# Kernel optimization log

Measured on AMD Instinct MI355X. Metric: run time of the kernel, lower is better.

## Reference

```python
import jax, jax.numpy as jnp
import numpy as np

NUM_SPLITS = 2  # attn_splits


def _split_c_last(x, ns):
    # split_feature(channel_last=True): [b,h,w,c] -> [b*ns*ns, h/ns, w/ns, c]
    b, h, w, c = x.shape
    x = x.reshape(b, ns, h // ns, ns, w // ns, c)
    x = jnp.transpose(x, (0, 1, 3, 2, 4, 5))
    return x.reshape(b * ns * ns, h // ns, w // ns, c)


def _merge_c_last(x, ns):
    # merge_splits(channel_last=True): [b*ns*ns, hh, ww, c] -> [b, ns*hh, ns*ww, c]
    bn, hh, ww, c = x.shape
    b = bn // (ns * ns)
    x = x.reshape(b, ns, ns, hh, ww, c)
    x = jnp.transpose(x, (0, 1, 3, 2, 4, 5))
    return x.reshape(b, ns * hh, ns * ww, c)


def _make_shift_window_mask(h, w, ns):
    # exact port of generate_shift_window_attn_mask (numpy, setup-time only)
    wh, ww = h // ns, w // ns
    sh, sw = wh // 2, ww // 2
    img = np.zeros((h, w))
    cnt = 0
    for hs in (slice(0, -wh), slice(-wh, -sh), slice(-sh, None)):
        for ws in (slice(0, -ww), slice(-ww, -sw), slice(-sw, None)):
            img[hs, ws] = cnt
            cnt += 1
    mw = img.reshape(ns, wh, ns, ww).transpose(0, 2, 1, 3).reshape(ns * ns, wh * ww)
    am = mw[:, None, :] - mw[:, :, None]  # [n, i, j] = mw[n, j] - mw[n, i]
    am = np.where(am != 0, -100.0, 0.0).astype(np.float32)
    return jnp.asarray(am)


def _window_attention(q, k, v, attn_mask, h, w, ns):
    # single_head_split_window_attention with with_shift=True
    b, hw, c = q.shape
    sh, sw = (h // ns) // 2, (w // ns) // 2

    def prep(x):
        x = x.reshape(b, h, w, c)
        x = jnp.roll(x, shift=(-sh, -sw), axis=(1, 2))
        return _split_c_last(x, ns).reshape(b * ns * ns, -1, c)

    qs, ks, vs = prep(q), prep(k), prep(v)
    scale = jnp.asarray(c, q.dtype) ** 0.5
    scores = jnp.einsum('bqc,bkc->bqk', qs, ks) / scale
    scores = scores + jnp.tile(attn_mask, (b, 1, 1))
    attn = jax.nn.softmax(scores, axis=-1)
    out = jnp.einsum('bqk,bkc->bqc', attn, vs)
    out = _merge_c_last(out.reshape(b * ns * ns, h // ns, w // ns, c), ns)
    out = jnp.roll(out, shift=(sh, sw), axis=(1, 2))
    return out.reshape(b, hw, c)


def _global_correlation_softmax(feature0, feature1):
    b, c, h, w = feature0.shape
    hw = h * w
    f0 = feature0.reshape(b, c, hw).transpose(0, 2, 1)  # [b, hw, c]
    f1 = feature1.reshape(b, c, hw)                     # [b, c, hw]
    scale = jnp.asarray(c, feature0.dtype) ** 0.5
    corr = jnp.matmul(f0, f1) / scale                   # [b, hw, hw]

    yy, xx = jnp.meshgrid(jnp.arange(h), jnp.arange(w), indexing='ij')
    init_grid = jnp.stack([xx, yy], axis=0).astype(feature0.dtype)  # [2,h,w]
    init_grid = jnp.broadcast_to(init_grid[None], (b, 2, h, w))
    grid = init_grid.reshape(b, 2, hw).transpose(0, 2, 1)            # [b, hw, 2]

    corr2 = jnp.concatenate([corr, jnp.transpose(corr, (0, 2, 1))], axis=0)  # [2b,hw,hw]
    grid2 = jnp.tile(grid, (2, 1, 1))
    init2 = jnp.tile(init_grid, (2, 1, 1, 1))

    prob = jax.nn.softmax(corr2, axis=-1)
    corresp = jnp.matmul(prob, grid2).reshape(2 * b, h, w, 2)
    corresp = jnp.transpose(corresp, (0, 3, 1, 2))
    flow = corresp - init2
    f01, f10 = flow[:b], flow[b:]
    dual_prob = prob[:b] * jnp.transpose(prob[b:], (0, 2, 1))
    return f01, f10, dual_prob


def setup_inputs() -> dict:
    key = jax.random.key(0)
    b, c, h, w = 2, 128, 48, 96
    ks = jax.random.split(key, 5)
    q = jax.random.normal(ks[0], (b, h * w, c), dtype=jnp.float32)
    k = jax.random.normal(ks[1], (b, h * w, c), dtype=jnp.float32)
    v = jax.random.normal(ks[2], (b, h * w, c), dtype=jnp.float32)
    feature0 = jax.random.normal(ks[3], (b, c, h, w), dtype=jnp.float32)
    feature1 = jax.random.normal(ks[4], (b, c, h, w), dtype=jnp.float32)
    attn_mask = _make_shift_window_mask(h, w, NUM_SPLITS)
    return {"q": q, "k": k, "v": v, "feature0": feature0, "feature1": feature1,
            "attn_mask": attn_mask, "h": h, "w": w}


def reference(q, k, v, feature0, feature1, attn_mask, h, w):
    attn_out = _window_attention(q, k, v, attn_mask, h, w, NUM_SPLITS)
    f01, f10, dual_prob = _global_correlation_softmax(feature0, feature1)
    return (attn_out, f01, f10, dual_prob)
```

## Files before the change

kernel.cpp:

```cpp
#include <hip/hip_runtime.h>

#define HW 4608
#define CC 128
#define H 48
#define W 96
#define S_WIN 1152
#define SCALE 0.08838834764831845f

typedef __attribute__((ext_vector_type(8))) short bf16x8;
typedef __attribute__((ext_vector_type(4))) float f32x4;

static __device__ inline short f2bf(float f) {
    unsigned u = __builtin_bit_cast(unsigned, f);
    unsigned r = (u + 0x7fff + ((u >> 16) & 1)) >> 16;
    return (short)r;
}

__global__ __launch_bounds__(256)
void prep_corr(const float* __restrict__ f0, const float* __restrict__ f1,
               bf16x8* __restrict__ fragA, bf16x8* __restrict__ fragB)
{
    __shared__ float vt[32][68];
    const int t = threadIdx.x;
    const int pt = blockIdx.x;
    const int z  = blockIdx.y;
    const int tensor = z >> 3, b = (z >> 2) & 1, kc = z & 3;
    const float* src = (tensor ? f1 : f0) + (size_t)b * CC * HW + (size_t)kc * 32 * HW + pt * 64;
    {
        int ch = t >> 4;
        int c4 = (t & 15) * 4;
        *(float4*)&vt[ch][c4]      = *(const float4*)&src[(size_t)ch * HW + c4];
        *(float4*)&vt[ch + 16][c4] = *(const float4*)&src[(size_t)(ch + 16) * HW + c4];
    }
    __syncthreads();
    int Rloc = t >> 6, lane = t & 63;
    int R = pt * 4 + Rloc;
    bf16x8 v;
    #pragma unroll
    for (int j = 0; j < 8; ++j) v[j] = f2bf(vt[(lane >> 4) * 8 + j][Rloc * 16 + (lane & 15)]);
    (tensor ? fragB : fragA)[((size_t)(b * 288 + R) * 4 + kc) * 64 + lane] = v;
}

__global__ __launch_bounds__(256)
void prep_qkv(const float* __restrict__ Q, const float* __restrict__ K, const float* __restrict__ V,
              bf16x8* __restrict__ qfrag, bf16x8* __restrict__ kfrag, bf16x8* __restrict__ vfrag)
{
    __shared__ float vt[32][132];
    const int t  = threadIdx.x;
    const int R2 = blockIdx.x;
    const int z  = blockIdx.y;
    const int tensor = z >> 3, wb = z & 7;
    const int bb = wb >> 2, wi = wb & 3, si = wi >> 1, sj = wi & 1;
    const float* src = (tensor == 0 ? Q : (tensor == 1 ? K : V)) + (size_t)bb * HW * CC;
    {
        int row = t >> 3;
        int c16 = (t & 7) * 16;
        int qw = R2 * 32 + row;
        int rr = qw / 48, cc = qw - rr * 48;
        int y = (si * 24 + rr + 12) % 48;
        int x = (sj * 48 + cc + 24) % 96;
        const float* rp = src + ((size_t)y * 96 + x) * CC + c16;
        #pragma unroll
        for (int u = 0; u < 4; ++u)
            *(float4*)&vt[row][c16 + u * 4] = *(const float4*)&rp[u * 4];
    }
    __syncthreads();
    if (tensor < 2) {
        bf16x8* frag = tensor == 0 ? qfrag : kfrag;
        #pragma unroll
        for (int e2 = 0; e2 < 2; ++e2) {
            int e = t + e2 * 256;
            int Rloc = e >> 8, kc = (e >> 6) & 3, lane = e & 63;
            int R = R2 * 2 + Rloc;
            bf16x8 v;
            #pragma unroll
            for (int j = 0; j < 8; ++j)
                v[j] = f2bf(vt[Rloc * 16 + (lane & 15)][kc * 32 + (lane >> 4) * 8 + j]);
            frag[((size_t)(wb * 72 + R) * 4 + kc) * 64 + lane] = v;
        }
    } else {
        #pragma unroll
        for (int e2 = 0; e2 < 2; ++e2) {
            int e = t + e2 * 256;
            int dB = e >> 6, lane = e & 63;
            bf16x8 v;
            #pragma unroll
            for (int j = 0; j < 8; ++j)
                v[j] = f2bf(vt[(lane >> 4) * 8 + j][dB * 16 + (lane & 15)]);
            vfrag[((size_t)(wb * 8 + dB) * 36 + R2) * 64 + lane] = v;
        }
    }
}

__global__ __launch_bounds__(512)
void win_attn(const bf16x8* __restrict__ qfrag, const bf16x8* __restrict__ kfrag,
              const bf16x8* __restrict__ vfrag, float* __restrict__ out)
{
    __shared__ __align__(16) short Psh[32 * 1152];
    __shared__ unsigned char codes[S_WIN];
    __shared__ float rsum_sh[32];

    const int t = threadIdx.x, lane = t & 63, w = t >> 6;
    const int qt = blockIdx.x, wb = blockIdx.y;
    const int bb = wb >> 2, wi = wb & 3, si = wi >> 1, sj = wi & 1;

    if (t < 32) rsum_sh[t] = 0.f;
    for (int i = t; i < S_WIN; i += 512) {
        int r = i / 48, c = i - r * 48;
        int rb = si ? (r >= 12) : 0;
        int cb = sj ? (c >= 24) : 0;
        codes[i] = (unsigned char)(rb | (cb << 1));
    }
    __syncthreads();

    bf16x8 qf[2][4];
    {
        const bf16x8* qb = qfrag + ((size_t)(wb * 72 + qt * 2) * 4) * 64 + lane;
        #pragma unroll
        for (int qh = 0; qh < 2; ++qh)
            #pragma unroll
            for (int kc = 0; kc < 4; ++kc) qf[qh][kc] = qb[(qh * 4 + kc) * 64];
    }
    int qcode[2];
    qcode[0] = codes[qt * 32 + (lane & 15)];
    qcode[1] = codes[qt * 32 + 16 + (lane & 15)];

    char* Pb = (char*)Psh;
    float rsum[2] = {0.f, 0.f};

    for (int kt = 0; kt < 9; ++kt) {
        int Rk = w * 9 + kt;
        bf16x8 kf[4];
        const bf16x8* kb = kfrag + ((size_t)(wb * 72 + Rk) * 4) * 64 + lane;
        #pragma unroll
        for (int kc = 0; kc < 4; ++kc) kf[kc] = kb[kc * 64];
        int k0 = Rk * 16 + (lane >> 4) * 4;
        int kcd[4];
        #pragma unroll
        for (int r = 0; r < 4; ++r) kcd[r] = codes[k0 + r];
        #pragma unroll
        for (int qh = 0; qh < 2; ++qh) {
            f32x4 acc = {0.f, 0.f, 0.f, 0.f};
            #pragma unroll
            for (int kc = 0; kc < 4; ++kc)
                acc = __builtin_amdgcn_mfma_f32_16x16x32_bf16(kf[kc], qf[qh][kc], acc, 0, 0, 0);
            float ev[4];
            #pragma unroll
            for (int r = 0; r < 4; ++r) {
                ev[r] = (kcd[r] == qcode[qh]) ? __expf(acc[r] * SCALE) : 0.f;
                rsum[qh] += ev[r];
            }
            unsigned lo = (unsigned)(unsigned short)f2bf(ev[0]) | ((unsigned)(unsigned short)f2bf(ev[1]) << 16);
            unsigned hi = (unsigned)(unsigned short)f2bf(ev[2]) | ((unsigned)(unsigned short)f2bf(ev[3]) << 16);
            int qloc = qh * 16 + (lane & 15);
            int off = (qloc * 2304 + k0 * 2) ^ ((qloc & 7) << 4);
            *(uint2*)(Pb + off) = make_uint2(lo, hi);
        }
    }
    #pragma unroll
    for (int qh = 0; qh < 2; ++qh) {
        float s = rsum[qh];
        s += __shfl_xor(s, 16); s += __shfl_xor(s, 32);
        if (lane < 16) atomicAdd(&rsum_sh[qh * 16 + lane], s);
    }
    __syncthreads();

    f32x4 pv[2] = {};
    const bf16x8* vb = vfrag + ((size_t)(wb * 8 + w) * 36) * 64 + lane;
    for (int kc = 0; kc < 36; ++kc) {
        bf16x8 vf = vb[kc * 64];
        #pragma unroll
        for (int qh = 0; qh < 2; ++qh) {
            int qloc = qh * 16 + (lane & 15);
            int off = (qloc * 2304 + kc * 64 + (lane >> 4) * 16) ^ ((qloc & 7) << 4);
            bf16x8 pf = *(const bf16x8*)(Pb + off);
            pv[qh] = __builtin_amdgcn_mfma_f32_16x16x32_bf16(pf, vf, pv[qh], 0, 0, 0);
        }
    }
    #pragma unroll
    for (int qh = 0; qh < 2; ++qh) {
        #pragma unroll
        for (int r = 0; r < 4; ++r) {
            int qloc = qh * 16 + (lane >> 4) * 4 + r;
            float val = pv[qh][r] / rsum_sh[qloc];
            int qw = qt * 32 + qloc;
            int rr = qw / 48, cc2 = qw - rr * 48;
            int y = (si * 24 + rr + 12) % 48;
            int x = (sj * 48 + cc2 + 24) % 96;
            out[((size_t)bb * HW + y * 96 + x) * CC + w * 16 + (lane & 15)] = val;
        }
    }
}

__global__ __launch_bounds__(256)
void corr_stats(const bf16x8* __restrict__ fragA, const bf16x8* __restrict__ fragB,
                float* __restrict__ rowsum, float* __restrict__ colsum)
{
    __shared__ float rs[128], cs[128];
    const int t = threadIdx.x, lane = t & 63, wave = t >> 6;
    const int wm = wave >> 1, wn = wave & 1;
    const int kt = blockIdx.x, qt = blockIdx.y, b = blockIdx.z;

    const bf16x8* Ab = fragA + (size_t)(b * 288 + qt * 8 + wm * 4) * 256 + lane;
    const bf16x8* Bb = fragB + (size_t)(b * 288 + kt * 8 + wn * 4) * 256 + lane;

    f32x4 acc[4][4] = {};
    #pragma unroll
    for (int kc = 0; kc < 4; ++kc) {
        bf16x8 a[4], bf[4];
        #pragma unroll
        for (int m = 0; m < 4; ++m) a[m]  = Ab[(m * 4 + kc) * 64];
        #pragma unroll
        for (int n = 0; n < 4; ++n) bf[n] = Bb[(n * 4 + kc) * 64];
        #pragma unroll
        for (int m = 0; m < 4; ++m)
            #pragma unroll
            for (int n = 0; n < 4; ++n)
                acc[m][n] = __builtin_amdgcn_mfma_f32_16x16x32_bf16(a[m], bf[n], acc[m][n], 0, 0, 0);
    }

    if (t < 128) { rs[t] = 0.f; cs[t] = 0.f; }
    __syncthreads();

    float cv[4] = {};
    #pragma unroll
    for (int m = 0; m < 4; ++m) {
        float rv[4] = {};
        #pragma unroll
        for (int n = 0; n < 4; ++n)
            #pragma unroll
            for (int r = 0; r < 4; ++r) {
                float ev = __expf(acc[m][n][r] * SCALE);
                rv[r] += ev; cv[n] += ev;
            }
        #pragma unroll
        for (int r = 0; r < 4; ++r) {
            float s = rv[r];
            s += __shfl_xor(s, 1); s += __shfl_xor(s, 2);
            s += __shfl_xor(s, 4); s += __shfl_xor(s, 8);
            if ((lane & 15) == 0)
                atomicAdd(&rs[wm * 64 + m * 16 + (lane >> 4) * 4 + r], s);
        }
    }
    #pragma unroll
    for (int n = 0; n < 4; ++n) {
        float s = cv[n];
        s += __shfl_xor(s, 16); s += __shfl_xor(s, 32);
        if (lane < 16) atomicAdd(&cs[wn * 64 + n * 16 + lane], s);
    }
    __syncthreads();
    if (t < 128)      atomicAdd(&rowsum[(size_t)b * HW + qt * 128 + t], rs[t]);
    else              atomicAdd(&colsum[(size_t)b * HW + kt * 128 + (t - 128)], cs[t - 128]);
}

__global__ __launch_bounds__(256)
void corr_final(const bf16x8* __restrict__ fragA, const bf16x8* __restrict__ fragB,
                const float* __restrict__ rowsum, const float* __restrict__ colsum,
                float* __restrict__ rowflow, float* __restrict__ colflow,
                float* __restrict__ dual)
{
    __shared__ float sfx[128], sfy[128], scx[128], scy[128];
    const int t = threadIdx.x, lane = t & 63, wave = t >> 6;
    const int wm = wave >> 1, wn = wave & 1;
    const int kt = blockIdx.x, qt = blockIdx.y, b = blockIdx.z;

    const bf16x8* Ab = fragA + (size_t)(b * 288 + qt * 8 + wm * 4) * 256 + lane;
    const bf16x8* Bb = fragB + (size_t)(b * 288 + kt * 8 + wn * 4) * 256 + lane;

    f32x4 acc[4][4] = {};
    #pragma unroll
    for (int kc = 0; kc < 4; ++kc) {
        bf16x8 a[4], bf[4];
        #pragma unroll
        for (int m = 0; m < 4; ++m) a[m]  = Ab[(m * 4 + kc) * 64];
        #pragma unroll
        for (int n = 0; n < 4; ++n) bf[n] = Bb[(n * 4 + kc) * 64];
        #pragma unroll
        for (int m = 0; m < 4; ++m)
            #pragma unroll
            for (int n = 0; n < 4; ++n)
                acc[m][n] = __builtin_amdgcn_mfma_f32_16x16x32_bf16(a[m], bf[n], acc[m][n], 0, 0, 0);
    }

    if (t < 128) { sfx[t] = 0.f; sfy[t] = 0.f; scx[t] = 0.f; scy[t] = 0.f; }
    __syncthreads();

    const int qbase = qt * 128 + wm * 64;
    const int kbase = kt * 128 + wn * 64;

    float cinv[4], gkx[4], gky[4];
    #pragma unroll
    for (int n = 0; n < 4; ++n) {
        int k = kbase + n * 16 + (lane & 15);
        cinv[n] = 1.f / colsum[(size_t)b * HW + k];
        int kyi = k / W;
        gkx[n] = (float)(k - kyi * W); gky[n] = (float)kyi;
    }

    float cfx[4] = {}, cfy[4] = {};
    #pragma unroll
    for (int m = 0; m < 4; ++m) {
        float rinv[4], gqx[4], gqy[4];
        int q0 = qbase + m * 16 + (lane >> 4) * 4;
        #pragma unroll
        for (int r = 0; r < 4; ++r) {
            rinv[r] = 1.f / rowsum[(size_t)b * HW + q0 + r];
            int qyi = (q0 + r) / W;
            gqx[r] = (float)(q0 + r - qyi * W); gqy[r] = (float)qyi;
        }
        float rfx[4] = {}, rfy[4] = {};
        #pragma unroll
        for (int n = 0; n < 4; ++n) {
            #pragma unroll
            for (int r = 0; r < 4; ++r) {
                float ev = __expf(acc[m][n][r] * SCALE);
                float rp = ev * rinv[r];
                float ce = ev * cinv[n];
                dual[((size_t)b * HW + q0 + r) * HW + kbase + n * 16 + (lane & 15)] = rp * ce;
                rfx[r] += rp * gkx[n]; rfy[r] += rp * gky[n];
                cfx[n] += ce * gqx[r]; cfy[n] += ce * gqy[r];
            }
        }
        #pragma unroll
        for (int r = 0; r < 4; ++r) {
            float sx = rfx[r], sy = rfy[r];
            sx += __shfl_xor(sx, 1); sx += __shfl_xor(sx, 2);
            sx += __shfl_xor(sx, 4); sx += __shfl_xor(sx, 8);
            sy += __shfl_xor(sy, 1); sy += __shfl_xor(sy, 2);
            sy += __shfl_xor(sy, 4); sy += __shfl_xor(sy, 8);
            if ((lane & 15) == 0) {
                int row = wm * 64 + m * 16 + (lane >> 4) * 4 + r;
                atomicAdd(&sfx[row], sx); atomicAdd(&sfy[row], sy);
            }
        }
    }
    #pragma unroll
    for (int n = 0; n < 4; ++n) {
        float sx = cfx[n], sy = cfy[n];
        sx += __shfl_xor(sx, 16); sx += __shfl_xor(sx, 32);
        sy += __shfl_xor(sy, 16); sy += __shfl_xor(sy, 32);
        if (lane < 16) {
            int col = wn * 64 + n * 16 + lane;
            atomicAdd(&scx[col], sx); atomicAdd(&scy[col], sy);
        }
    }
    __syncthreads();
    if (t < 128) {
        atomicAdd(&rowflow[((size_t)b * HW + qt * 128 + t) * 2 + 0], sfx[t]);
        atomicAdd(&rowflow[((size_t)b * HW + qt * 128 + t) * 2 + 1], sfy[t]);
    } else {
        int j = t - 128;
        atomicAdd(&colflow[((size_t)b * HW + kt * 128 + j) * 2 + 0], scx[j]);
        atomicAdd(&colflow[((size_t)b * HW + kt * 128 + j) * 2 + 1], scy[j]);
    }
}

__global__ void flow_finalize(const float* __restrict__ rowflow, const float* __restrict__ colflow,
                              float* __restrict__ out)
{
    int i = blockIdx.x * 256 + threadIdx.x;
    if (i >= 2 * 2 * HW) return;
    int bb   = i / (2 * HW);
    int rem  = i % (2 * HW);
    int chan = rem / HW;
    int q    = rem % HW;
    float g = (chan == 0) ? (float)(q % W) : (float)(q / W);
    out[i]              = rowflow[((size_t)bb * HW + q) * 2 + chan] - g;
    out[2 * 2 * HW + i] = colflow[((size_t)bb * HW + q) * 2 + chan] - g;
}

extern "C" void kernel_launch(void* const* d_in, const int* in_sizes, int n_in,
                              void* d_out, int out_size, void* d_ws, size_t ws_size,
                              hipStream_t stream)
{
    (void)in_sizes; (void)n_in; (void)out_size; (void)ws_size;
    const float* q    = (const float*)d_in[0];
    const float* k    = (const float*)d_in[1];
    const float* v    = (const float*)d_in[2];
    const float* f0   = (const float*)d_in[3];
    const float* f1   = (const float*)d_in[4];

    float* out = (float*)d_out;
    const size_t ATTN_SZ = (size_t)2 * HW * CC;
    const size_t FLOW_SZ = (size_t)2 * 2 * HW;
    float* f01  = out + ATTN_SZ;
    float* dual = out + ATTN_SZ + 2 * FLOW_SZ;

    const size_t FR = 2359296;
    char* wsb = (char*)d_ws;
    bf16x8* cfragA = (bf16x8*)(wsb);
    bf16x8* cfragB = (bf16x8*)(wsb + FR);
    bf16x8* qfrag  = (bf16x8*)(wsb + 2 * FR);
    bf16x8* kfrag  = (bf16x8*)(wsb + 3 * FR);
    bf16x8* vfrag  = (bf16x8*)(wsb + 4 * FR);
    float* wsf     = (float*)(wsb + 5 * FR);
    float* rowsum  = wsf;
    float* colsum  = wsf + 2 * HW;
    float* rowflow = wsf + 4 * HW;
    float* colflow = wsf + 8 * HW;
    hipMemsetAsync(wsf, 0, (size_t)12 * HW * sizeof(float), stream);

    prep_corr<<<dim3(72, 16), 256, 0, stream>>>(f0, f1, cfragA, cfragB);
    prep_qkv<<<dim3(36, 24), 256, 0, stream>>>(q, k, v, qfrag, kfrag, vfrag);
    win_attn<<<dim3(36, 8), 512, 0, stream>>>(qfrag, kfrag, vfrag, out);
    corr_stats<<<dim3(36, 36, 2), 256, 0, stream>>>(cfragA, cfragB, rowsum, colsum);
    corr_final<<<dim3(36, 36, 2), 256, 0, stream>>>(cfragA, cfragB, rowsum, colsum,
                                                    rowflow, colflow, dual);
    flow_finalize<<<dim3(72), 256, 0, stream>>>(rowflow, colflow, f01);
}
```

Baseline: 141.0 us.

## Fuse prep kernels with memset, split window attention finer, coalesce dual stores

Merges the two prep kernels and the workspace memset into one launch, which removes launch and memset overhead. Window attention now handles 16 queries per block instead of 32, doubling the grid to 576 blocks and halving LDS use, so more blocks can be resident. The cost is that K and V fragments are reloaded twice as often. The dual-probability output in corr_final is staged through shared memory so it can be written as coalesced float4 rows, replacing scattered scalar stores on the largest output.

```diff
diff --git a/kernel.cpp b/kernel.cpp
--- a/kernel.cpp
+++ b/kernel.cpp
@@ -17,77 +17,80 @@
 }
 
 __global__ __launch_bounds__(256)
-void prep_corr(const float* __restrict__ f0, const float* __restrict__ f1,
-               bf16x8* __restrict__ fragA, bf16x8* __restrict__ fragB)
-{
-    __shared__ float vt[32][68];
+void prep_all(const float* __restrict__ Q, const float* __restrict__ K, const float* __restrict__ V,
+              const float* __restrict__ f0, const float* __restrict__ f1,
+              bf16x8* __restrict__ cfragA, bf16x8* __restrict__ cfragB,
+              bf16x8* __restrict__ qfrag, bf16x8* __restrict__ kfrag, bf16x8* __restrict__ vfrag,
+              float* __restrict__ wsf)
+{
+    __shared__ float vt[32][132];
+    const int bx = blockIdx.x;
     const int t = threadIdx.x;
-    const int pt = blockIdx.x;
-    const int z  = blockIdx.y;
-    const int tensor = z >> 3, b = (z >> 2) & 1, kc = z & 3;
-    const float* src = (tensor ? f1 : f0) + (size_t)b * CC * HW + (size_t)kc * 32 * HW + pt * 64;
-    {
-        int ch = t >> 4;
-        int c4 = (t & 15) * 4;
-        *(float4*)&vt[ch][c4]      = *(const float4*)&src[(size_t)ch * HW + c4];
-        *(float4*)&vt[ch + 16][c4] = *(const float4*)&src[(size_t)(ch + 16) * HW + c4];
-    }
-    __syncthreads();
-    int Rloc = t >> 6, lane = t & 63;
-    int R = pt * 4 + Rloc;
-    bf16x8 v;
-    #pragma unroll
-    for (int j = 0; j < 8; ++j) v[j] = f2bf(vt[(lane >> 4) * 8 + j][Rloc * 16 + (lane & 15)]);
-    (tensor ? fragB : fragA)[((size_t)(b * 288 + R) * 4 + kc) * 64 + lane] = v;
-}
-
-__global__ __launch_bounds__(256)
-void prep_qkv(const float* __restrict__ Q, const float* __restrict__ K, const float* __restrict__ V,
-              bf16x8* __restrict__ qfrag, bf16x8* __restrict__ kfrag, bf16x8* __restrict__ vfrag)
-{
-    __shared__ float vt[32][132];
-    const int t  = threadIdx.x;
-    const int R2 = blockIdx.x;
-    const int z  = blockIdx.y;
-    const int tensor = z >> 3, wb = z & 7;
-    const int bb = wb >> 2, wi = wb & 3, si = wi >> 1, sj = wi & 1;
-    const float* src = (tensor == 0 ? Q : (tensor == 1 ? K : V)) + (size_t)bb * HW * CC;
-    {
-        int row = t >> 3;
-        int c16 = (t & 7) * 16;
-        int qw = R2 * 32 + row;
-        int rr = qw / 48, cc = qw - rr * 48;
-        int y = (si * 24 + rr + 12) % 48;
-        int x = (sj * 48 + cc + 24) % 96;
-        const float* rp = src + ((size_t)y * 96 + x) * CC + c16;
-        #pragma unroll
-        for (int u = 0; u < 4; ++u)
-            *(float4*)&vt[row][c16 + u * 4] = *(const float4*)&rp[u * 4];
-    }
-    __syncthreads();
-    if (tensor < 2) {
-        bf16x8* frag = tensor == 0 ? qfrag : kfrag;
-        #pragma unroll
-        for (int e2 = 0; e2 < 2; ++e2) {
-            int e = t + e2 * 256;
-            int Rloc = e >> 8, kc = (e >> 6) & 3, lane = e & 63;
-            int R = R2 * 2 + Rloc;
-            bf16x8 v;
-            #pragma unroll
-            for (int j = 0; j < 8; ++j)
-                v[j] = f2bf(vt[Rloc * 16 + (lane & 15)][kc * 32 + (lane >> 4) * 8 + j]);
-            frag[((size_t)(wb * 72 + R) * 4 + kc) * 64 + lane] = v;
-        }
+
+    if (bx < 1152) {
+        int zi = bx * 256 + t;
+        if (zi < 12 * HW) wsf[zi] = 0.f;
+        const int pt = bx % 72;
+        const int z  = bx / 72;
+        const int tensor = z >> 3, b = (z >> 2) & 1, kc = z & 3;
+        const float* src = (tensor ? f1 : f0) + (size_t)b * CC * HW + (size_t)kc * 32 * HW + pt * 64;
+        {
+            int ch = t >> 4;
+            int c4 = (t & 15) * 4;
+            *(float4*)&vt[ch][c4]      = *(const float4*)&src[(size_t)ch * HW + c4];
+            *(float4*)&vt[ch + 16][c4] = *(const float4*)&src[(size_t)(ch + 16) * HW + c4];
+        }
+        __syncthreads();
+        int Rloc = t >> 6, lane = t & 63;
+        int R = pt * 4 + Rloc;
+        bf16x8 v;
+        #pragma unroll
+        for (int j = 0; j < 8; ++j) v[j] = f2bf(vt[(lane >> 4) * 8 + j][Rloc * 16 + (lane & 15)]);
+        (tensor ? cfragB : cfragA)[((size_t)(b * 288 + R) * 4 + kc) * 64 + lane] = v;
     } else {
-        #pragma unroll
-        for (int e2 = 0; e2 < 2; ++e2) {
-            int e = t + e2 * 256;
-            int dB = e >> 6, lane = e & 63;
-            bf16x8 v;
-            #pragma unroll
-            for (int j = 0; j < 8; ++j)
-                v[j] = f2bf(vt[(lane >> 4) * 8 + j][dB * 16 + (lane & 15)]);
-            vfrag[((size_t)(wb * 8 + dB) * 36 + R2) * 64 + lane] = v;
+        const int bx2 = bx - 1152;
+        const int R2 = bx2 % 36;
+        const int z  = bx2 / 36;
+        const int tensor = z >> 3, wb = z & 7;
+        const int bb = wb >> 2, wi = wb & 3, si = wi >> 1, sj = wi & 1;
+        const float* src = (tensor == 0 ? Q : (tensor == 1 ? K : V)) + (size_t)bb * HW * CC;
+        {
+            int row = t >> 3;
+            int c16 = (t & 7) * 16;
+            int qw = R2 * 32 + row;
+            int rr = qw / 48, cc = qw - rr * 48;
+            int y = (si * 24 + rr + 12) % 48;
+            int x = (sj * 48 + cc + 24) % 96;
+            const float* rp = src + ((size_t)y * 96 + x) * CC + c16;
+            #pragma unroll
+            for (int u = 0; u < 4; ++u)
+                *(float4*)&vt[row][c16 + u * 4] = *(const float4*)&rp[u * 4];
+        }
+        __syncthreads();
+        if (tensor < 2) {
+            bf16x8* frag = tensor == 0 ? qfrag : kfrag;
+            #pragma unroll
+            for (int e2 = 0; e2 < 2; ++e2) {
+                int e = t + e2 * 256;
+                int Rloc = e >> 8, kc = (e >> 6) & 3, lane = e & 63;
+                int R = R2 * 2 + Rloc;
+                bf16x8 v;
+                #pragma unroll
+                for (int j = 0; j < 8; ++j)
+                    v[j] = f2bf(vt[Rloc * 16 + (lane & 15)][kc * 32 + (lane >> 4) * 8 + j]);
+                frag[((size_t)(wb * 72 + R) * 4 + kc) * 64 + lane] = v;
+            }
+        } else {
+            #pragma unroll
+            for (int e2 = 0; e2 < 2; ++e2) {
+                int e = t + e2 * 256;
+                int dB = e >> 6, lane = e & 63;
+                bf16x8 v;
+                #pragma unroll
+                for (int j = 0; j < 8; ++j)
+                    v[j] = f2bf(vt[(lane >> 4) * 8 + j][dB * 16 + (lane & 15)]);
+                vfrag[((size_t)(wb * 8 + dB) * 36 + R2) * 64 + lane] = v;
+            }
         }
     }
 }
@@ -96,99 +99,76 @@
 void win_attn(const bf16x8* __restrict__ qfrag, const bf16x8* __restrict__ kfrag,
               const bf16x8* __restrict__ vfrag, float* __restrict__ out)
 {
-    __shared__ __align__(16) short Psh[32 * 1152];
+    __shared__ __align__(16) short Psh[16 * 1152];
     __shared__ unsigned char codes[S_WIN];
-    __shared__ float rsum_sh[32];
+    __shared__ float rsum_sh[16];
 
     const int t = threadIdx.x, lane = t & 63, w = t >> 6;
-    const int qt = blockIdx.x, wb = blockIdx.y;
+    const int qt = blockIdx.x;
+    const int wb = blockIdx.y;
     const int bb = wb >> 2, wi = wb & 3, si = wi >> 1, sj = wi & 1;
 
-    if (t < 32) rsum_sh[t] = 0.f;
+    if (t < 16) rsum_sh[t] = 0.f;
     for (int i = t; i < S_WIN; i += 512) {
         int r = i / 48, c = i - r * 48;
-        int rb = si ? (r >= 12) : 0;
-        int cb = sj ? (c >= 24) : 0;
-        codes[i] = (unsigned char)(rb | (cb << 1));
-    }
-    __syncthreads();
-
-    bf16x8 qf[2][4];
+        codes[i] = (unsigned char)((si ? (r >= 12) : 0) | ((sj ? (c >= 24) : 0) << 1));
+    }
+    __syncthreads();
+
+    bf16x8 qf[4];
     {
-        const bf16x8* qb = qfrag + ((size_t)(wb * 72 + qt * 2) * 4) * 64 + lane;
-        #pragma unroll
-        for (int qh = 0; qh < 2; ++qh)
-            #pragma unroll
-            for (int kc = 0; kc < 4; ++kc) qf[qh][kc] = qb[(qh * 4 + kc) * 64];
-    }
-    int qcode[2];
-    qcode[0] = codes[qt * 32 + (lane & 15)];
-    qcode[1] = codes[qt * 32 + 16 + (lane & 15)];
-
+        const bf16x8* qb = qfrag + ((size_t)(wb * 72 + qt) * 4) * 64 + lane;
+        #pragma unroll
+        for (int kc = 0; kc < 4; ++kc) qf[kc] = qb[kc * 64];
+    }
+    const int qcode = codes[qt * 16 + (lane & 15)];
     char* Pb = (char*)Psh;
-    float rsum[2] = {0.f, 0.f};
+    float rsum = 0.f;
 
     for (int kt = 0; kt < 9; ++kt) {
         int Rk = w * 9 + kt;
+        const bf16x8* kb = kfrag + ((size_t)(wb * 72 + Rk) * 4) * 64 + lane;
         bf16x8 kf[4];
-        const bf16x8* kb = kfrag + ((size_t)(wb * 72 + Rk) * 4) * 64 + lane;
         #pragma unroll
         for (int kc = 0; kc < 4; ++kc) kf[kc] = kb[kc * 64];
         int k0 = Rk * 16 + (lane >> 4) * 4;
-        int kcd[4];
-        #pragma unroll
-        for (int r = 0; r < 4; ++r) kcd[r] = codes[k0 + r];
-        #pragma unroll
-        for (int qh = 0; qh < 2; ++qh) {
-            f32x4 acc = {0.f, 0.f, 0.f, 0.f};
-            #pragma unroll
-            for (int kc = 0; kc < 4; ++kc)
-                acc = __builtin_amdgcn_mfma_f32_16x16x32_bf16(kf[kc], qf[qh][kc], acc, 0, 0, 0);
-            float ev[4];
-            #pragma unroll
-            for (int r = 0; r < 4; ++r) {
-                ev[r] = (kcd[r] == qcode[qh]) ? __expf(acc[r] * SCALE) : 0.f;
-                rsum[qh] += ev[r];
-            }
-            unsigned lo = (unsigned)(unsigned short)f2bf(ev[0]) | ((unsigned)(unsigned short)f2bf(ev[1]) << 16);
-            unsigned hi = (unsigned)(unsigned short)f2bf(ev[2]) | ((unsigned)(unsigned short)f2bf(ev[3]) << 16);
-            int qloc = qh * 16 + (lane & 15);
-            int off = (qloc * 2304 + k0 * 2) ^ ((qloc & 7) << 4);
-            *(uint2*)(Pb + off) = make_uint2(lo, hi);
-        }
-    }
-    #pragma unroll
-    for (int qh = 0; qh < 2; ++qh) {
-        float s = rsum[qh];
-        s += __shfl_xor(s, 16); s += __shfl_xor(s, 32);
-        if (lane < 16) atomicAdd(&rsum_sh[qh * 16 + lane], s);
-    }
-    __syncthreads();
-
-    f32x4 pv[2] = {};
+        f32x4 acc = {0.f, 0.f, 0.f, 0.f};
+        #pragma unroll
+        for (int kc = 0; kc < 4; ++kc)
+            acc = __builtin_amdgcn_mfma_f32_16x16x32_bf16(kf[kc], qf[kc], acc, 0, 0, 0);
+        float ev[4];
+        #pragma unroll
+        for (int r = 0; r < 4; ++r) {
+            ev[r] = (codes[k0 + r] == qcode) ? __expf(acc[r] * SCALE) : 0.f;
+            rsum += ev[r];
+        }
+        unsigned lo = (unsigned)(unsigned short)f2bf(ev[0]) | ((unsigned)(unsigned short)f2bf(ev[1]) << 16);
+        unsigned hi = (unsigned)(unsigned short)f2bf(ev[2]) | ((unsigned)(unsigned short)f2bf(ev[3]) << 16);
+        int qloc = lane & 15;
+        int off = (qloc * 2304 + k0 * 2) ^ ((qloc & 7) << 4);
+        *(uint2*)(Pb + off) = make_uint2(lo, hi);
+    }
+    rsum += __shfl_xor(rsum, 16); rsum += __shfl_xor(rsum, 32);
+    if (lane < 16) atomicAdd(&rsum_sh[lane], rsum);
+    __syncthreads();
+
+    f32x4 pv = {0.f, 0.f, 0.f, 0.f};
     const bf16x8* vb = vfrag + ((size_t)(wb * 8 + w) * 36) * 64 + lane;
     for (int kc = 0; kc < 36; ++kc) {
-        bf16x8 vf = vb[kc * 64];
-        #pragma unroll
-        for (int qh = 0; qh < 2; ++qh) {
-            int qloc = qh * 16 + (lane & 15);
-            int off = (qloc * 2304 + kc * 64 + (lane >> 4) * 16) ^ ((qloc & 7) << 4);
-            bf16x8 pf = *(const bf16x8*)(Pb + off);
-            pv[qh] = __builtin_amdgcn_mfma_f32_16x16x32_bf16(pf, vf, pv[qh], 0, 0, 0);
-        }
-    }
-    #pragma unroll
-    for (int qh = 0; qh < 2; ++qh) {
-        #pragma unroll
-        for (int r = 0; r < 4; ++r) {
-            int qloc = qh * 16 + (lane >> 4) * 4 + r;
-            float val = pv[qh][r] / rsum_sh[qloc];
-            int qw = qt * 32 + qloc;
-            int rr = qw / 48, cc2 = qw - rr * 48;
-            int y = (si * 24 + rr + 12) % 48;
-            int x = (sj * 48 + cc2 + 24) % 96;
-            out[((size_t)bb * HW + y * 96 + x) * CC + w * 16 + (lane & 15)] = val;
-        }
+        int qloc = lane & 15;
+        int off = (qloc * 2304 + kc * 64 + (lane >> 4) * 16) ^ ((qloc & 7) << 4);
+        bf16x8 pf = *(const bf16x8*)(Pb + off);
+        pv = __builtin_amdgcn_mfma_f32_16x16x32_bf16(pf, vb[kc * 64], pv, 0, 0, 0);
+    }
+    #pragma unroll
+    for (int r = 0; r < 4; ++r) {
+        int qloc = (lane >> 4) * 4 + r;
+        float val = pv[r] / rsum_sh[qloc];
+        int qw = qt * 16 + qloc;
+        int rr = qw / 48, cc2 = qw - rr * 48;
+        int y = (si * 24 + rr + 12) % 48;
+        int x = (sj * 48 + cc2 + 24) % 96;
+        out[((size_t)bb * HW + y * 96 + x) * CC + w * 16 + (lane & 15)] = val;
     }
 }
 
@@ -260,6 +240,7 @@
                 float* __restrict__ dual)
 {
     __shared__ float sfx[128], sfy[128], scx[128], scy[128];
+    __shared__ float stg[4][16][68];
     const int t = threadIdx.x, lane = t & 63, wave = t >> 6;
     const int wm = wave >> 1, wn = wave & 1;
     const int kt = blockIdx.x, qt = blockIdx.y, b = blockIdx.z;
@@ -316,10 +297,16 @@
                 float ev = __expf(acc[m][n][r] * SCALE);
                 float rp = ev * rinv[r];
                 float ce = ev * cinv[n];
-                dual[((size_t)b * HW + q0 + r) * HW + kbase + n * 16 + (lane & 15)] = rp * ce;
+                stg[wave][(lane >> 4) * 4 + r][n * 16 + (lane & 15)] = rp * ce;
                 rfx[r] += rp * gkx[n]; rfy[r] += rp * gky[n];
                 cfx[n] += ce * gqx[r]; cfy[n] += ce * gqy[r];
             }
+        }
+        #pragma unroll
+        for (int pass = 0; pass < 4; ++pass) {
+            int row = pass * 4 + (lane >> 4);
+            float4 vv = *(const float4*)&stg[wave][row][(lane & 15) * 4];
+            *(float4*)&dual[((size_t)b * HW + qbase + m * 16 + row) * HW + kbase + (lane & 15) * 4] = vv;
         }
         #pragma unroll
         for (int r = 0; r < 4; ++r) {
@@ -374,11 +361,11 @@
                               hipStream_t stream)
 {
     (void)in_sizes; (void)n_in; (void)out_size; (void)ws_size;
-    const float* q    = (const float*)d_in[0];
-    const float* k    = (const float*)d_in[1];
-    const float* v    = (const float*)d_in[2];
-    const float* f0   = (const float*)d_in[3];
-    const float* f1   = (const float*)d_in[4];
+    const float* q  = (const float*)d_in[0];
+    const float* k  = (const float*)d_in[1];
+    const float* v  = (const float*)d_in[2];
+    const float* f0 = (const float*)d_in[3];
+    const float* f1 = (const float*)d_in[4];
 
     float* out = (float*)d_out;
     const size_t ATTN_SZ = (size_t)2 * HW * CC;
@@ -398,11 +385,10 @@
     float* colsum  = wsf + 2 * HW;
     float* rowflow = wsf + 4 * HW;
     float* colflow = wsf + 8 * HW;
-    hipMemsetAsync(wsf, 0, (size_t)12 * HW * sizeof(float), stream);
-
-    prep_corr<<<dim3(72, 16), 256, 0, stream>>>(f0, f1, cfragA, cfragB);
-    prep_qkv<<<dim3(36, 24), 256, 0, stream>>>(q, k, v, qfrag, kfrag, vfrag);
-    win_attn<<<dim3(36, 8), 512, 0, stream>>>(qfrag, kfrag, vfrag, out);
+
+    prep_all<<<dim3(2016), 256, 0, stream>>>(q, k, v, f0, f1, cfragA, cfragB,
+                                             qfrag, kfrag, vfrag, wsf);
+    win_attn<<<dim3(72, 8), 512, 0, stream>>>(qfrag, kfrag, vfrag, out);
     corr_stats<<<dim3(36, 36, 2), 256, 0, stream>>>(cfragA, cfragB, rowsum, colsum);
     corr_final<<<dim3(36, 36, 2), 256, 0, stream>>>(cfragA, cfragB, rowsum, colsum,
                                                     rowflow, colflow, dual);
```

Measured after the change: 133.8 us. 1.05x faster.
